# Kernel optimization log

Hardware: AMD Instinct MI355X
Metric: run time of the kernel (lower is better)

The kernel has to match this reference:

```python
import jax, jax.numpy as jnp
import numpy as np

B, D, T, H = 2048, 512, 16, 1024   # batch, covariate_dim, treatment_dim, mlp hidden
K, M = 50, 16                       # k_neighbors, manifold_dim


def _mlp(xt, W1, b1, W2, b2):
    # outcome model: [B, D+T] -> [B, 1]
    return jnp.tanh(xt @ W1 + b1) @ W2 + b2


def setup_inputs() -> dict:
    key = jax.random.key(0)
    k0, k1, k2, k3, k4 = jax.random.split(key, 5)
    x = jax.random.normal(k0, (B, D), dtype=jnp.float32)
    t = jax.random.normal(k1, (B, T), dtype=jnp.float32)
    perturbations = jax.random.normal(k2, (B, D), dtype=jnp.float32)
    W1 = jax.random.normal(k3, (D + T, H), dtype=jnp.float32) / np.float32(np.sqrt(D + T))
    b1 = jnp.zeros((H,), dtype=jnp.float32)
    W2 = jax.random.normal(k4, (H, 1), dtype=jnp.float32) / np.float32(np.sqrt(H))
    b2 = jnp.zeros((1,), dtype=jnp.float32)
    return {"x": x, "t": t, "perturbations": perturbations,
            "W1": W1, "b1": b1, "W2": W2, "b2": b2}


def reference(x, t, perturbations, W1, b1, W2, b2):
    # grad of sum(y) w.r.t. x (create_graph analog handled by composing jax.grad)
    def scalar_out(xx):
        return _mlp(jnp.concatenate([xx, t], axis=-1), W1, b1, W2, b2).sum()
    grad_x = jax.grad(scalar_out)(x)                      # [B, D]

    # kNN on perturbations (squared distances preserve topk-smallest ordering)
    sq = jnp.sum(perturbations * perturbations, axis=-1)  # [B]
    d2 = sq[:, None] + sq[None, :] - 2.0 * (perturbations @ perturbations.T)
    _, idx = jax.lax.top_k(-d2, K)                        # [B, K] nearest (incl. self)

    neigh = perturbations[idx]                            # [B, K, D] gather
    centered = neigh - neigh.mean(axis=1, keepdims=True)
    # batched reduced SVD: Vt has shape [B, min(K,D), D]
    _, _, Vt = jnp.linalg.svd(centered, full_matrices=False)
    basis = jnp.swapaxes(Vt[:, :M, :], 1, 2)              # [B, D, M] top-M right sing. vecs

    # projection of grad onto tangent space, summed squared norm
    coef = jnp.einsum('bdm,bd->bm', basis, grad_x)        # [B, M]
    proj = jnp.einsum('bdm,bm->bd', basis, coef)          # [B, D]
    return jnp.sum(proj * proj) / B
```

## Files before the change

### kernel.cpp

```cpp
#include <hip/hip_runtime.h>
#include <math.h>
#include <float.h>

#define B_ 2048
#define D_ 512
#define T_ 16
#define H_ 1024
#define K_ 50
#define M_ 16
#define NSWEEP 1
#define SX_STRIDE 2656
#define SLAB 128
#define SROW 136
#define FS 52

typedef __attribute__((ext_vector_type(8))) short s16x8;
typedef __attribute__((ext_vector_type(4))) float f32x4;
typedef __attribute__((ext_vector_type(2))) float f32x2;

#define GLL16(g, l) __builtin_amdgcn_global_load_lds( \
    (const __attribute__((address_space(1))) void*)(g), \
    (__attribute__((address_space(3))) void*)(l), 16, 0, 0)

__device__ __forceinline__ float bsum64(float v) {
  #pragma unroll
  for (int o = 1; o < 64; o <<= 1) v += __shfl_xor(v, o);
  return v;
}

__device__ __forceinline__ unsigned bf16_rne(float v) {
  union { float f; unsigned u; } a; a.f = v;
  return (a.u + 0x7FFFu + ((a.u >> 16) & 1u)) >> 16;
}
__device__ __forceinline__ float bf16_val(unsigned h) {
  union { unsigned u; float f; } a; a.u = h << 16;
  return a.f;
}
__device__ __forceinline__ void split_bf16(float v, unsigned short* h, unsigned short* l) {
  unsigned hh = bf16_rne(v);
  *h = (unsigned short)hh;
  *l = (unsigned short)bf16_rne(v - bf16_val(hh));
}

__global__ __launch_bounds__(256)
void prep_conv(const float* __restrict__ x, const float* __restrict__ t,
               const float* __restrict__ P, const float* __restrict__ W1,
               unsigned short* __restrict__ xh, unsigned short* __restrict__ xl,
               unsigned short* __restrict__ ph, unsigned short* __restrict__ pl,
               float* __restrict__ sq,
               unsigned short* __restrict__ th, unsigned short* __restrict__ tl,
               unsigned short* __restrict__ wh, unsigned short* __restrict__ wl,
               float* __restrict__ out) {
  __shared__ float tile[32][33];
  __shared__ float red[4];
  const int bid = blockIdx.x, tid = threadIdx.x;
  if (bid < B_) {
    const int b = bid;
    if (b == 0 && tid == 0) out[0] = 0.f;
    for (int c = tid; c < 544; c += 256) {
      float v = 0.f;
      if (c < 512) v = x[(size_t)b * 512 + c];
      else if (c < 528) v = t[(size_t)b * 16 + (c - 512)];
      unsigned short hh, ll; split_bf16(v, &hh, &ll);
      xh[(size_t)b * 544 + c] = hh;
      xl[(size_t)b * 544 + c] = ll;
    }
    float s = 0.f;
    for (int c = tid; c < 512; c += 256) {
      float v = P[(size_t)b * 512 + c];
      s += v * v;
      unsigned short hh, ll; split_bf16(v, &hh, &ll);
      ph[(size_t)b * 512 + c] = hh;
      pl[(size_t)b * 512 + c] = ll;
    }
    s = bsum64(s);
    if ((tid & 63) == 0) red[tid >> 6] = s;
    __syncthreads();
    if (tid == 0) sq[b] = (red[0] + red[1]) + (red[2] + red[3]);
  } else {
    const int cid = bid - B_;
    const int tx = tid & 31, ty = tid >> 5;
    const int kb = (cid % 17) * 32, hb = (cid / 17) * 32;
    #pragma unroll
    for (int j = 0; j < 4; j++) {
      int k = kb + ty + j * 8;
      float v = (k < 528) ? W1[(size_t)k * 1024 + hb + tx] : 0.f;
      tile[ty + j * 8][tx] = v;
      if (k < 528) {
        unsigned short hh, ll; split_bf16(v, &hh, &ll);
        wh[(size_t)k * 1024 + hb + tx] = hh;
        wl[(size_t)k * 1024 + hb + tx] = ll;
      }
    }
    __syncthreads();
    #pragma unroll
    for (int j = 0; j < 4; j++) {
      int hrow = hb + ty + j * 8;
      float v = tile[tx][ty + j * 8];
      unsigned short hh, ll; split_bf16(v, &hh, &ll);
      th[(size_t)hrow * 544 + kb + tx] = hh;
      tl[(size_t)hrow * 544 + kb + tx] = ll;
    }
  }
}

template <int EPI, int PASSES>
__global__ __launch_bounds__(256)
void mfma_nt(const unsigned short* __restrict__ Ah, const unsigned short* __restrict__ Al, int lda,
             const unsigned short* __restrict__ Bh, const unsigned short* __restrict__ Bl, int ldb,
             int K, float* __restrict__ C, int ldc,
             const float* __restrict__ b1, const float* __restrict__ W2,
             unsigned short* __restrict__ acth, unsigned short* __restrict__ actl) {
  __shared__ unsigned short sAh[2 * 2048], sBh[2 * 2048];
  __shared__ unsigned short sAl[PASSES == 3 ? 2 * 2048 : 16];
  __shared__ unsigned short sBl[PASSES == 3 ? 2 * 2048 : 16];
  const int tid = threadIdx.x;
  const int lane = tid & 63, wv = tid >> 6;
  const int wm = wv >> 1, wn = wv & 1;
  const int lr = lane & 15, lq = lane >> 4;
  const int m0 = blockIdx.y * 64, n0 = blockIdx.x * 64;
  const int srow = wv * 16 + (lane >> 2);
  const int sx = (srow & 3) ^ ((srow >> 2) & 3);
  const int gch = ((lane & 3) ^ sx) * 8;
  const size_t rowA = (size_t)(m0 + srow) * lda + gch;
  const size_t rowB = (size_t)(n0 + srow) * ldb + gch;

  f32x4 acc[2][2];
  #pragma unroll
  for (int mt = 0; mt < 2; mt++)
    #pragma unroll
    for (int nt = 0; nt < 2; nt++)
      #pragma unroll
      for (int i = 0; i < 4; i++) acc[mt][nt][i] = 0.f;

  auto STAGE = [&](int bufi, int kb) {
    const int off = bufi * 2048 + wv * 512;
    GLL16(Ah + rowA + kb, &sAh[off]);
    GLL16(Bh + rowB + kb, &sBh[off]);
    if (PASSES == 3) {
      GLL16(Al + rowA + kb, &sAl[off]);
      GLL16(Bl + rowB + kb, &sBl[off]);
    }
  };

  auto COMPUTE = [&](int bufi) {
    const int bo = bufi * 2048;
    s16x8 fah[2], fal[2], fbh[2], fbl[2];
    #pragma unroll
    for (int mt = 0; mt < 2; mt++) {
      const int r = wm * 32 + mt * 16 + lr;
      const int xo = (lq ^ ((r & 3) ^ ((r >> 2) & 3))) * 8;
      fah[mt] = *(const s16x8*)&sAh[bo + r * 32 + xo];
      if (PASSES == 3) fal[mt] = *(const s16x8*)&sAl[bo + r * 32 + xo];
    }
    #pragma unroll
    for (int nt = 0; nt < 2; nt++) {
      const int r = wn * 32 + nt * 16 + lr;
      const int xo = (lq ^ ((r & 3) ^ ((r >> 2) & 3))) * 8;
      fbh[nt] = *(const s16x8*)&sBh[bo + r * 32 + xo];
      if (PASSES == 3) fbl[nt] = *(const s16x8*)&sBl[bo + r * 32 + xo];
    }
    #pragma unroll
    for (int mt = 0; mt < 2; mt++)
      #pragma unroll
      for (int nt = 0; nt < 2; nt++)
        acc[mt][nt] = __builtin_amdgcn_mfma_f32_16x16x32_bf16(fah[mt], fbh[nt], acc[mt][nt], 0, 0, 0);
    if (PASSES == 3) {
      #pragma unroll
      for (int mt = 0; mt < 2; mt++)
        #pragma unroll
        for (int nt = 0; nt < 2; nt++)
          acc[mt][nt] = __builtin_amdgcn_mfma_f32_16x16x32_bf16(fah[mt], fbl[nt], acc[mt][nt], 0, 0, 0);
      #pragma unroll
      for (int mt = 0; mt < 2; mt++)
        #pragma unroll
        for (int nt = 0; nt < 2; nt++)
          acc[mt][nt] = __builtin_amdgcn_mfma_f32_16x16x32_bf16(fal[mt], fbh[nt], acc[mt][nt], 0, 0, 0);
    }
  };

  STAGE(0, 0);
  __syncthreads();
  int cur = 0;
  for (int kb = 32; kb < K; kb += 32) {
    STAGE(cur ^ 1, kb);
    COMPUTE(cur);
    __syncthreads();
    cur ^= 1;
  }
  COMPUTE(cur);

  #pragma unroll
  for (int nt = 0; nt < 2; nt++) {
    const int n = n0 + wn * 32 + nt * 16 + lr;
    float bb = 0.f, ww = 0.f;
    if (EPI == 1) { bb = b1[n]; ww = W2[n]; }
    #pragma unroll
    for (int mt = 0; mt < 2; mt++) {
      #pragma unroll
      for (int r = 0; r < 4; r++) {
        const int m = m0 + wm * 32 + mt * 16 + lq * 4 + r;
        float v = acc[mt][nt][r];
        if (EPI == 0) {
          C[(size_t)m * ldc + n] = v;
        } else if (EPI == 1) {
          float z = v + bb;
          float e = __builtin_amdgcn_exp2f(fabsf(z) * -2.885390082f);
          float rc = __builtin_amdgcn_rcpf(1.f + e);
          float s = 4.f * e * rc * rc * ww;
          unsigned short hh, ll; split_bf16(s, &hh, &ll);
          acth[(size_t)m * ldc + n] = hh;
          actl[(size_t)m * ldc + n] = ll;
        } else {
          unsigned short hh, ll; split_bf16(v, &hh, &ll);
          acth[(size_t)m * ldc + n] = hh;
          actl[(size_t)m * ldc + n] = ll;
        }
      }
    }
  }
}

__global__ __launch_bounds__(256)
void sbuild_kernel(const unsigned short* __restrict__ ph, const unsigned short* __restrict__ pl,
                   const unsigned short* __restrict__ gh, const unsigned short* __restrict__ gl,
                   const int* __restrict__ idx, float* __restrict__ Sx) {
  __shared__ unsigned short sh[64 * SROW];
  __shared__ unsigned short sl[64 * SROW];
  __shared__ int ids[K_];
  const int b = blockIdx.x;
  const int tid = threadIdx.x;
  if (tid < K_) ids[tid] = idx[b * K_ + tid];
  const int lane = tid & 63, wv = tid >> 6;
  const int wm = wv >> 1, wn = wv & 1;
  const int lr = lane & 15, lq = lane >> 4;
  const int strow = tid >> 4, stk = (tid & 15) * 8;
  __syncthreads();

  f32x4 acc[2][2];
  #pragma unroll
  for (int mt = 0; mt < 2; mt++)
    #pragma unroll
    for (int nt = 0; nt < 2; nt++)
      #pragma unroll
      for (int i = 0; i < 4; i++) acc[mt][nt][i] = 0.f;

  for (int kb = 0; kb < 512; kb += SLAB) {
    __syncthreads();
    #pragma unroll
    for (int p = 0; p < 4; p++) {
      const int r = p * 16 + strow;
      if (r < 51) {
        const unsigned short* srch = (r < 50) ? ph + (size_t)ids[r] * 512 : gh + (size_t)b * 512;
        const unsigned short* srcl = (r < 50) ? pl + (size_t)ids[r] * 512 : gl + (size_t)b * 512;
        *(float4*)&sh[r * SROW + stk] = *(const float4*)(srch + kb + stk);
        *(float4*)&sl[r * SROW + stk] = *(const float4*)(srcl + kb + stk);
      }
    }
    __syncthreads();
    #pragma unroll
    for (int kk = 0; kk < SLAB; kk += 32) {
      s16x8 fah[2], fal[2], fbh[2], fbl[2];
      #pragma unroll
      for (int mt = 0; mt < 2; mt++) {
        const int r = wm * 32 + mt * 16 + lr;
        fah[mt] = *(const s16x8*)&sh[r * SROW + kk + lq * 8];
        fal[mt] = *(const s16x8*)&sl[r * SROW + kk + lq * 8];
      }
      #pragma unroll
      for (int nt = 0; nt < 2; nt++) {
        const int r = wn * 32 + nt * 16 + lr;
        fbh[nt] = *(const s16x8*)&sh[r * SROW + kk + lq * 8];
        fbl[nt] = *(const s16x8*)&sl[r * SROW + kk + lq * 8];
      }
      #pragma unroll
      for (int mt = 0; mt < 2; mt++)
        #pragma unroll
        for (int nt = 0; nt < 2; nt++)
          acc[mt][nt] = __builtin_amdgcn_mfma_f32_16x16x32_bf16(fah[mt], fbh[nt], acc[mt][nt], 0, 0, 0);
      #pragma unroll
      for (int mt = 0; mt < 2; mt++)
        #pragma unroll
        for (int nt = 0; nt < 2; nt++)
          acc[mt][nt] = __builtin_amdgcn_mfma_f32_16x16x32_bf16(fah[mt], fbl[nt], acc[mt][nt], 0, 0, 0);
      #pragma unroll
      for (int mt = 0; mt < 2; mt++)
        #pragma unroll
        for (int nt = 0; nt < 2; nt++)
          acc[mt][nt] = __builtin_amdgcn_mfma_f32_16x16x32_bf16(fal[mt], fbh[nt], acc[mt][nt], 0, 0, 0);
    }
  }

  float* Sb = Sx + (size_t)b * SX_STRIDE;
  #pragma unroll
  for (int nt = 0; nt < 2; nt++) {
    const int n = wn * 32 + nt * 16 + lr;
    #pragma unroll
    for (int mt = 0; mt < 2; mt++) {
      #pragma unroll
      for (int r = 0; r < 4; r++) {
        const int m = wm * 32 + mt * 16 + lq * 4 + r;
        if (m < 51 && n < 52) Sb[m * 52 + n] = acc[mt][nt][r];
      }
    }
  }
}

__device__ __forceinline__ unsigned fkey(float f) {
  unsigned u = __float_as_uint(f);
  return u ^ ((unsigned)((int)u >> 31) | 0x80000000u);
}

__global__ __launch_bounds__(64)
void topk_kernel(const float* __restrict__ G, const float* __restrict__ sq,
                 int* __restrict__ idx) {
  const int b = blockIdx.x, lane = threadIdx.x;
  const float* row = G + (size_t)b * 2048;
  unsigned k[32];
  #pragma unroll
  for (int i = 0; i < 32; i++) {
    const int j = i * 64 + lane;
    k[i] = fkey(sq[j] - 2.f * row[j]);
  }
  unsigned V = 0;
  bool exact = false;
  for (int bit = 31; bit >= 0; bit--) {
    const unsigned cand = V | (1u << bit);
    int cnt = 0;
    #pragma unroll
    for (int i = 0; i < 32; i++) cnt += (k[i] < cand) ? 1 : 0;
    #pragma unroll
    for (int o = 1; o < 64; o <<= 1) cnt += __shfl_xor(cnt, o);
    if (cnt == K_) { V = cand; exact = true; break; }
    if (cnt < K_ + 1) V = cand;
  }
  int base = 0;
  #pragma unroll
  for (int i = 0; i < 32; i++) {
    const bool p = (k[i] < V);
    const unsigned long long mask = __ballot(p);
    if (p) {
      const int pos = base + __popcll(mask & ((1ull << lane) - 1ull));
      idx[b * K_ + pos] = i * 64 + lane;
    }
    base += __popcll(mask);
  }
  if (!exact && base < K_) {
    #pragma unroll
    for (int i = 0; i < 32; i++) {
      if (base >= K_) break;
      const bool p = (k[i] == V);
      const unsigned long long mask = __ballot(p);
      if (p) {
        const int pos = base + __popcll(mask & ((1ull << lane) - 1ull));
        if (pos < K_) idx[b * K_ + pos] = i * 64 + lane;
      }
      base += __popcll(mask);
    }
  }
}

__global__ __launch_bounds__(64, 2)
void final_kernel(const float* __restrict__ Sx, float* __restrict__ out) {
  __shared__ float cols[64 * FS];
  const int b = blockIdx.x;
  const int lane = threadIdx.x;
  const float* Sb = Sx + (size_t)b * SX_STRIDE;
  const bool act = lane < K_;

  float q = act ? Sb[50 * 52 + lane] : 0.f;
  float qm = bsum64(q) * (1.f / K_);
  float w = act ? (q - qm) : 0.f;

  f32x2 f2[25];
  #pragma unroll
  for (int i = 0; i < 25; i++) {
    f2[i].x = act ? Sb[(2 * i) * 52 + lane] : 0.f;
    f2[i].y = act ? Sb[(2 * i + 1) * 52 + lane] : 0.f;
  }

  float cm = 0.f;
  #pragma unroll
  for (int i = 0; i < 25; i++) cm += f2[i].x + f2[i].y;
  cm *= (1.f / K_);
  float gs = bsum64(act ? cm : 0.f) * (1.f / K_);
  float cs = cm - gs;
  #pragma unroll
  for (int i = 0; i < 25; i++) {
    float r0 = __shfl(cm, 2 * i);
    float r1 = __shfl(cm, 2 * i + 1);
    if (act) { f2[i].x -= r0 + cs; f2[i].y -= r1 + cs; }
  }

  float nrm = 0.f;
  #pragma unroll
  for (int i = 0; i < 25; i++) nrm += f2[i].x * f2[i].x + f2[i].y * f2[i].y;

  f32x4 f4[13];
  #pragma unroll
  for (int k = 0; k < 12; k++) {
    f4[k].x = f2[2 * k].x;     f4[k].y = f2[2 * k].y;
    f4[k].z = f2[2 * k + 1].x; f4[k].w = f2[2 * k + 1].y;
  }
  f4[12].x = f2[24].x; f4[12].y = f2[24].y; f4[12].z = nrm; f4[12].w = w;

  float* my = &cols[lane * FS];
  if (act) {
    #pragma unroll
    for (int k = 0; k < 13; k++) *(f32x4*)&my[4 * k] = f4[k];
  }

  for (int sweep = 0; sweep < NSWEEP; sweep++) {
    int mm = (lane == 0) ? 0 : 49 - lane;
    int kkv = 0;
    for (int r = 0; r < 49; r++) {
      if (act) {
        int m = mm;
        if (lane == kkv) m = 49;
        if (lane == 49)  m = kkv;

        const float* pc = &cols[m * FS];
        f32x4 y4[13];
        #pragma unroll
        for (int k = 0; k < 13; k++) y4[k] = *(const f32x4*)&pc[4 * k];
        const float onrm = y4[12].z;
        const float yw   = y4[12].w;

        f32x4 acc4 = {0.f, 0.f, 0.f, 0.f};
        #pragma unroll
        for (int k = 0; k < 12; k++) acc4 = __builtin_elementwise_fma(f4[k], y4[k], acc4);
        acc4.x = fmaf(f4[12].x, y4[12].x, acc4.x);
        acc4.y = fmaf(f4[12].y, y4[12].y, acc4.y);
        const float dot = (acc4.x + acc4.y) + (acc4.z + acc4.w);

        const bool isp = lane < m;
        float alpha = isp ? nrm : onrm;
        float beta  = isp ? onrm : nrm;
        float tau = (beta - alpha) * 0.5f * __builtin_amdgcn_rcpf(dot);
        float sg = (tau >= 0.f) ? 1.f : -1.f;
        float s1 = __builtin_amdgcn_sqrtf(1.f + tau * tau);
        float tt = sg * __builtin_amdgcn_rcpf(fabsf(tau) + s1);
        float cc = __builtin_amdgcn_rsqf(1.f + tt * tt);
        float ssv = tt * cc;
        float sr = isp ? -ssv : ssv;
        if (fabsf(dot) < 1e-20f) { cc = 1.f; sr = 0.f; }

        f32x4 c4 = {cc, cc, cc, cc};
        f32x4 s4 = {sr, sr, sr, sr};
        #pragma unroll
        for (int k = 0; k < 13; k++)
          f4[k] = __builtin_elementwise_fma(c4, f4[k], s4 * y4[k]);
        w = cc * w + sr * yw;
        nrm = cc * cc * nrm + sr * sr * onrm + 2.f * cc * sr * dot;
        f4[12].z = nrm;
        f4[12].w = w;

        #pragma unroll
        for (int k = 0; k < 13; k++) *(f32x4*)&my[4 * k] = f4[k];
      }
      mm = (mm == 48) ? 0 : mm + 1;
      kkv += 25; if (kkv >= 49) kkv -= 49;
    }
  }

  float n2 = 0.f;
  #pragma unroll
  for (int k = 0; k < 12; k++)
    n2 += f4[k].x * f4[k].x + f4[k].y * f4[k].y + f4[k].z * f4[k].z + f4[k].w * f4[k].w;
  n2 += f4[12].x * f4[12].x + f4[12].y * f4[12].y;
  int rank = 0;
  #pragma unroll
  for (int j = 0; j < K_; j++) {
    float vj = __shfl(n2, j);
    rank += (vj > n2 || (vj == n2 && j < lane)) ? 1 : 0;
  }
  float lam = sqrtf(n2);
  float contrib = (act && rank < M_) ? (w * w / lam) : 0.f;
  contrib = bsum64(contrib);
  if (lane == 0) atomicAdd(out, contrib * (1.f / B_));
}

extern "C" void kernel_launch(void* const* d_in, const int* in_sizes, int n_in,
                              void* d_out, int out_size, void* d_ws, size_t ws_size,
                              hipStream_t stream) {
  const float* x  = (const float*)d_in[0];
  const float* t  = (const float*)d_in[1];
  const float* P  = (const float*)d_in[2];
  const float* W1 = (const float*)d_in[3];
  const float* b1 = (const float*)d_in[4];
  const float* W2 = (const float*)d_in[5];
  float* out = (float*)d_out;

  float* G    = (float*)d_ws;
  float* Sx   = (float*)d_ws;
  unsigned short* xt_h  = (unsigned short*)(G + (size_t)B_ * B_);
  unsigned short* xt_l  = xt_h  + (size_t)B_ * 544;
  unsigned short* w1t_h = xt_l  + (size_t)B_ * 544;
  unsigned short* w1t_l = w1t_h + (size_t)H_ * 544;
  unsigned short* w1_h  = w1t_l + (size_t)H_ * 544;
  unsigned short* w1_l  = w1_h  + (size_t)528 * H_;
  unsigned short* p_h   = w1_l  + (size_t)528 * H_;
  unsigned short* p_l   = p_h   + (size_t)B_ * D_;
  unsigned short* act_h = p_l   + (size_t)B_ * D_;
  unsigned short* act_l = act_h + (size_t)B_ * H_;
  unsigned short* g_h   = act_l + (size_t)B_ * H_;
  unsigned short* g_l   = g_h   + (size_t)B_ * D_;
  float* sq   = (float*)(g_l + (size_t)B_ * D_);
  int*   idx  = (int*)(sq + B_);

  prep_conv<<<B_ + 544, 256, 0, stream>>>(x, t, P, W1, xt_h, xt_l, p_h, p_l, sq,
                                          w1t_h, w1t_l, w1_h, w1_l, out);

  mfma_nt<1, 3><<<dim3(H_ / 64, B_ / 64), 256, 0, stream>>>(
      xt_h, xt_l, 544, w1t_h, w1t_l, 544, 544,
      nullptr, H_, b1, W2, act_h, act_l);
  mfma_nt<2, 3><<<dim3(D_ / 64, B_ / 64), 256, 0, stream>>>(
      act_h, act_l, H_, w1_h, w1_l, H_, H_,
      nullptr, D_, nullptr, nullptr, g_h, g_l);
  mfma_nt<0, 1><<<dim3(B_ / 64, B_ / 64), 256, 0, stream>>>(
      p_h, nullptr, D_, p_h, nullptr, D_, D_,
      G, B_, nullptr, nullptr, nullptr, nullptr);

  topk_kernel<<<B_, 64, 0, stream>>>(G, sq, idx);
  sbuild_kernel<<<B_, 256, 0, stream>>>(p_h, p_l, g_h, g_l, idx, Sx);
  final_kernel<<<B_, 64, 0, stream>>>(Sx, out);
}
```

Baseline: 247.9 us.

## Fuse top-k into final kernel and gather Gram entries from full 3-pass P·Pᵀ

```diff
diff --git a/kernel.cpp b/kernel.cpp
--- a/kernel.cpp
+++ b/kernel.cpp
@@ -9,9 +9,6 @@
 #define K_ 50
 #define M_ 16
 #define NSWEEP 1
-#define SX_STRIDE 2656
-#define SLAB 128
-#define SROW 136
 #define FS 52
 
 typedef __attribute__((ext_vector_type(8))) short s16x8;
@@ -104,13 +101,14 @@
   }
 }
 
-template <int EPI, int PASSES>
+template <int EPI, int PASSES, int DUAL>
 __global__ __launch_bounds__(256)
 void mfma_nt(const unsigned short* __restrict__ Ah, const unsigned short* __restrict__ Al, int lda,
              const unsigned short* __restrict__ Bh, const unsigned short* __restrict__ Bl, int ldb,
              int K, float* __restrict__ C, int ldc,
              const float* __restrict__ b1, const float* __restrict__ W2,
-             unsigned short* __restrict__ acth, unsigned short* __restrict__ actl) {
+             unsigned short* __restrict__ acth, unsigned short* __restrict__ actl,
+             float* __restrict__ C1) {
   __shared__ unsigned short sAh[2 * 2048], sBh[2 * 2048];
   __shared__ unsigned short sAl[PASSES == 3 ? 2 * 2048 : 16];
   __shared__ unsigned short sBl[PASSES == 3 ? 2 * 2048 : 16];
@@ -126,12 +124,21 @@
   const size_t rowB = (size_t)(n0 + srow) * ldb + gch;
 
   f32x4 acc[2][2];
+  f32x4 acc1[DUAL ? 2 : 1][DUAL ? 2 : 1];
   #pragma unroll
   for (int mt = 0; mt < 2; mt++)
     #pragma unroll
     for (int nt = 0; nt < 2; nt++)
       #pragma unroll
       for (int i = 0; i < 4; i++) acc[mt][nt][i] = 0.f;
+  if (DUAL) {
+    #pragma unroll
+    for (int mt = 0; mt < 2; mt++)
+      #pragma unroll
+      for (int nt = 0; nt < 2; nt++)
+        #pragma unroll
+        for (int i = 0; i < 4; i++) acc1[mt][nt][i] = 0.f;
+  }
 
   auto STAGE = [&](int bufi, int kb) {
     const int off = bufi * 2048 + wv * 512;
@@ -165,6 +172,13 @@
       #pragma unroll
       for (int nt = 0; nt < 2; nt++)
         acc[mt][nt] = __builtin_amdgcn_mfma_f32_16x16x32_bf16(fah[mt], fbh[nt], acc[mt][nt], 0, 0, 0);
+    if (DUAL) {
+      #pragma unroll
+      for (int mt = 0; mt < 2; mt++)
+        #pragma unroll
+        for (int nt = 0; nt < 2; nt++)
+          acc1[mt][nt] = __builtin_amdgcn_mfma_f32_16x16x32_bf16(fah[mt], fbh[nt], acc1[mt][nt], 0, 0, 0);
+    }
     if (PASSES == 3) {
       #pragma unroll
       for (int mt = 0; mt < 2; mt++)
@@ -203,6 +217,7 @@
         float v = acc[mt][nt][r];
         if (EPI == 0) {
           C[(size_t)m * ldc + n] = v;
+          if (DUAL) C1[(size_t)m * ldc + n] = acc1[mt][nt][r];
         } else if (EPI == 1) {
           float z = v + bb;
           float e = __builtin_amdgcn_exp2f(fabsf(z) * -2.885390082f);
@@ -211,96 +226,7 @@
           unsigned short hh, ll; split_bf16(s, &hh, &ll);
           acth[(size_t)m * ldc + n] = hh;
           actl[(size_t)m * ldc + n] = ll;
-        } else {
-          unsigned short hh, ll; split_bf16(v, &hh, &ll);
-          acth[(size_t)m * ldc + n] = hh;
-          actl[(size_t)m * ldc + n] = ll;
         }
-      }
-    }
-  }
-}
-
-__global__ __launch_bounds__(256)
-void sbuild_kernel(const unsigned short* __restrict__ ph, const unsigned short* __restrict__ pl,
-                   const unsigned short* __restrict__ gh, const unsigned short* __restrict__ gl,
-                   const int* __restrict__ idx, float* __restrict__ Sx) {
-  __shared__ unsigned short sh[64 * SROW];
-  __shared__ unsigned short sl[64 * SROW];
-  __shared__ int ids[K_];
-  const int b = blockIdx.x;
-  const int tid = threadIdx.x;
-  if (tid < K_) ids[tid] = idx[b * K_ + tid];
-  const int lane = tid & 63, wv = tid >> 6;
-  const int wm = wv >> 1, wn = wv & 1;
-  const int lr = lane & 15, lq = lane >> 4;
-  const int strow = tid >> 4, stk = (tid & 15) * 8;
-  __syncthreads();
-
-  f32x4 acc[2][2];
-  #pragma unroll
-  for (int mt = 0; mt < 2; mt++)
-    #pragma unroll
-    for (int nt = 0; nt < 2; nt++)
-      #pragma unroll
-      for (int i = 0; i < 4; i++) acc[mt][nt][i] = 0.f;
-
-  for (int kb = 0; kb < 512; kb += SLAB) {
-    __syncthreads();
-    #pragma unroll
-    for (int p = 0; p < 4; p++) {
-      const int r = p * 16 + strow;
-      if (r < 51) {
-        const unsigned short* srch = (r < 50) ? ph + (size_t)ids[r] * 512 : gh + (size_t)b * 512;
-        const unsigned short* srcl = (r < 50) ? pl + (size_t)ids[r] * 512 : gl + (size_t)b * 512;
-        *(float4*)&sh[r * SROW + stk] = *(const float4*)(srch + kb + stk);
-        *(float4*)&sl[r * SROW + stk] = *(const float4*)(srcl + kb + stk);
-      }
-    }
-    __syncthreads();
-    #pragma unroll
-    for (int kk = 0; kk < SLAB; kk += 32) {
-      s16x8 fah[2], fal[2], fbh[2], fbl[2];
-      #pragma unroll
-      for (int mt = 0; mt < 2; mt++) {
-        const int r = wm * 32 + mt * 16 + lr;
-        fah[mt] = *(const s16x8*)&sh[r * SROW + kk + lq * 8];
-        fal[mt] = *(const s16x8*)&sl[r * SROW + kk + lq * 8];
-      }
-      #pragma unroll
-      for (int nt = 0; nt < 2; nt++) {
-        const int r = wn * 32 + nt * 16 + lr;
-        fbh[nt] = *(const s16x8*)&sh[r * SROW + kk + lq * 8];
-        fbl[nt] = *(const s16x8*)&sl[r * SROW + kk + lq * 8];
-      }
-      #pragma unroll
-      for (int mt = 0; mt < 2; mt++)
-        #pragma unroll
-        for (int nt = 0; nt < 2; nt++)
-          acc[mt][nt] = __builtin_amdgcn_mfma_f32_16x16x32_bf16(fah[mt], fbh[nt], acc[mt][nt], 0, 0, 0);
-      #pragma unroll
-      for (int mt = 0; mt < 2; mt++)
-        #pragma unroll
-        for (int nt = 0; nt < 2; nt++)
-          acc[mt][nt] = __builtin_amdgcn_mfma_f32_16x16x32_bf16(fah[mt], fbl[nt], acc[mt][nt], 0, 0, 0);
-      #pragma unroll
-      for (int mt = 0; mt < 2; mt++)
-        #pragma unroll
-        for (int nt = 0; nt < 2; nt++)
-          acc[mt][nt] = __builtin_amdgcn_mfma_f32_16x16x32_bf16(fal[mt], fbh[nt], acc[mt][nt], 0, 0, 0);
-    }
-  }
-
-  float* Sb = Sx + (size_t)b * SX_STRIDE;
-  #pragma unroll
-  for (int nt = 0; nt < 2; nt++) {
-    const int n = wn * 32 + nt * 16 + lr;
-    #pragma unroll
-    for (int mt = 0; mt < 2; mt++) {
-      #pragma unroll
-      for (int r = 0; r < 4; r++) {
-        const int m = wm * 32 + mt * 16 + lq * 4 + r;
-        if (m < 51 && n < 52) Sb[m * 52 + n] = acc[mt][nt][r];
       }
     }
   }
@@ -311,16 +237,29 @@
   return u ^ ((unsigned)((int)u >> 31) | 0x80000000u);
 }
 
-__global__ __launch_bounds__(64)
-void topk_kernel(const float* __restrict__ G, const float* __restrict__ sq,
-                 int* __restrict__ idx) {
-  const int b = blockIdx.x, lane = threadIdx.x;
-  const float* row = G + (size_t)b * 2048;
-  unsigned k[32];
+__global__ __launch_bounds__(64, 2)
+void final_kernel(const float* __restrict__ G1, const float* __restrict__ G3,
+                  const float* __restrict__ sq,
+                  const float* __restrict__ P, const float* __restrict__ g32,
+                  float* __restrict__ out) {
+  __shared__ float cols[64 * FS];
+  __shared__ float gld[512];
+  __shared__ int ids[64];
+  const int b = blockIdx.x;
+  const int lane = threadIdx.x;
+
+  {
+    const float4* grow = (const float4*)(g32 + (size_t)b * 512);
+    ((float4*)gld)[lane] = grow[lane];
+    ((float4*)gld)[lane + 64] = grow[lane + 64];
+  }
+
+  const float* row = G1 + (size_t)b * 2048;
+  unsigned kk[32];
   #pragma unroll
   for (int i = 0; i < 32; i++) {
     const int j = i * 64 + lane;
-    k[i] = fkey(sq[j] - 2.f * row[j]);
+    kk[i] = fkey(sq[j] - 2.f * row[j]);
   }
   unsigned V = 0;
   bool exact = false;
@@ -328,7 +267,7 @@
     const unsigned cand = V | (1u << bit);
     int cnt = 0;
     #pragma unroll
-    for (int i = 0; i < 32; i++) cnt += (k[i] < cand) ? 1 : 0;
+    for (int i = 0; i < 32; i++) cnt += (kk[i] < cand) ? 1 : 0;
     #pragma unroll
     for (int o = 1; o < 64; o <<= 1) cnt += __shfl_xor(cnt, o);
     if (cnt == K_) { V = cand; exact = true; break; }
@@ -337,11 +276,11 @@
   int base = 0;
   #pragma unroll
   for (int i = 0; i < 32; i++) {
-    const bool p = (k[i] < V);
+    const bool p = (kk[i] < V);
     const unsigned long long mask = __ballot(p);
     if (p) {
       const int pos = base + __popcll(mask & ((1ull << lane) - 1ull));
-      idx[b * K_ + pos] = i * 64 + lane;
+      ids[pos] = i * 64 + lane;
     }
     base += __popcll(mask);
   }
@@ -349,34 +288,42 @@
     #pragma unroll
     for (int i = 0; i < 32; i++) {
       if (base >= K_) break;
-      const bool p = (k[i] == V);
+      const bool p = (kk[i] == V);
       const unsigned long long mask = __ballot(p);
       if (p) {
         const int pos = base + __popcll(mask & ((1ull << lane) - 1ull));
-        if (pos < K_) idx[b * K_ + pos] = i * 64 + lane;
+        if (pos < K_) ids[pos] = i * 64 + lane;
       }
       base += __popcll(mask);
     }
   }
-}
-
-__global__ __launch_bounds__(64, 2)
-void final_kernel(const float* __restrict__ Sx, float* __restrict__ out) {
-  __shared__ float cols[64 * FS];
-  const int b = blockIdx.x;
-  const int lane = threadIdx.x;
-  const float* Sb = Sx + (size_t)b * SX_STRIDE;
+
   const bool act = lane < K_;
-
-  float q = act ? Sb[50 * 52 + lane] : 0.f;
-  float qm = bsum64(q) * (1.f / K_);
+  const int mycol = act ? ids[lane] : 0;
+
+  float q = 0.f;
+  if (act) {
+    const float4* Pr = (const float4*)(P + (size_t)mycol * 512);
+    f32x4 qa = {0.f, 0.f, 0.f, 0.f};
+    #pragma unroll 4
+    for (int c = 0; c < 128; c++) {
+      float4 pv = Pr[c];
+      float4 gv = ((const float4*)gld)[c];
+      qa.x = fmaf(gv.x, pv.x, qa.x);
+      qa.y = fmaf(gv.y, pv.y, qa.y);
+      qa.z = fmaf(gv.z, pv.z, qa.z);
+      qa.w = fmaf(gv.w, pv.w, qa.w);
+    }
+    q = (qa.x + qa.y) + (qa.z + qa.w);
+  }
+  float qm = bsum64(act ? q : 0.f) * (1.f / K_);
   float w = act ? (q - qm) : 0.f;
 
   f32x2 f2[25];
   #pragma unroll
   for (int i = 0; i < 25; i++) {
-    f2[i].x = act ? Sb[(2 * i) * 52 + lane] : 0.f;
-    f2[i].y = act ? Sb[(2 * i + 1) * 52 + lane] : 0.f;
+    f2[i].x = act ? G3[(size_t)ids[2 * i] * 2048 + mycol] : 0.f;
+    f2[i].y = act ? G3[(size_t)ids[2 * i + 1] * 2048 + mycol] : 0.f;
   }
 
   float cm = 0.f;
@@ -491,9 +438,10 @@
   const float* W2 = (const float*)d_in[5];
   float* out = (float*)d_out;
 
-  float* G    = (float*)d_ws;
-  float* Sx   = (float*)d_ws;
-  unsigned short* xt_h  = (unsigned short*)(G + (size_t)B_ * B_);
+  float* G3   = (float*)d_ws;
+  unsigned short* act_h = (unsigned short*)(G3 + (size_t)B_ * B_);
+  unsigned short* act_l = act_h + (size_t)B_ * H_;
+  unsigned short* xt_h  = act_l + (size_t)B_ * H_;
   unsigned short* xt_l  = xt_h  + (size_t)B_ * 544;
   unsigned short* w1t_h = xt_l  + (size_t)B_ * 544;
   unsigned short* w1t_l = w1t_h + (size_t)H_ * 544;
@@ -501,27 +449,22 @@
   unsigned short* w1_l  = w1_h  + (size_t)528 * H_;
   unsigned short* p_h   = w1_l  + (size_t)528 * H_;
   unsigned short* p_l   = p_h   + (size_t)B_ * D_;
-  unsigned short* act_h = p_l   + (size_t)B_ * D_;
-  unsigned short* act_l = act_h + (size_t)B_ * H_;
-  unsigned short* g_h   = act_l + (size_t)B_ * H_;
-  unsigned short* g_l   = g_h   + (size_t)B_ * D_;
-  float* sq   = (float*)(g_l + (size_t)B_ * D_);
-  int*   idx  = (int*)(sq + B_);
+  float* g32  = (float*)(p_l + (size_t)B_ * D_);
+  float* sq   = g32 + (size_t)B_ * D_;
+  float* G1   = (float*)act_h;
 
   prep_conv<<<B_ + 544, 256, 0, stream>>>(x, t, P, W1, xt_h, xt_l, p_h, p_l, sq,
                                           w1t_h, w1t_l, w1_h, w1_l, out);
 
-  mfma_nt<1, 3><<<dim3(H_ / 64, B_ / 64), 256, 0, stream>>>(
+  mfma_nt<1, 3, 0><<<dim3(H_ / 64, B_ / 64), 256, 0, stream>>>(
       xt_h, xt_l, 544, w1t_h, w1t_l, 544, 544,
-      nullptr, H_, b1, W2, act_h, act_l);
-  mfma_nt<2, 3><<<dim3(D_ / 64, B_ / 64), 256, 0, stream>>>(
+      nullptr, H_, b1, W2, act_h, act_l, nullptr);
+  mfma_nt<0, 3, 0><<<dim3(D_ / 64, B_ / 64), 256, 0, stream>>>(
       act_h, act_l, H_, w1_h, w1_l, H_, H_,
-      nullptr, D_, nullptr, nullptr, g_h, g_l);
-  mfma_nt<0, 1><<<dim3(B_ / 64, B_ / 64), 256, 0, stream>>>(
-      p_h, nullptr, D_, p_h, nullptr, D_, D_,
-      G, B_, nullptr, nullptr, nullptr, nullptr);
-
-  topk_kernel<<<B_, 64, 0, stream>>>(G, sq, idx);
-  sbuild_kernel<<<B_, 256, 0, stream>>>(p_h, p_l, g_h, g_l, idx, Sx);
-  final_kernel<<<B_, 64, 0, stream>>>(Sx, out);
-}
+      g32, D_, nullptr, nullptr, nullptr, nullptr, nullptr);
+  mfma_nt<0, 3, 1><<<dim3(B_ / 64, B_ / 64), 256, 0, stream>>>(
+      p_h, p_l, D_, p_h, p_l, D_, D_,
+      G3, B_, nullptr, nullptr, nullptr, nullptr, G1);
+
+  final_kernel<<<B_, 64, 0, stream>>>(G1, G3, sq, P, g32, out);
+}
```

New measurement: 245.3 us. No clear change (-1.0%).

## Merge independent activation GEMM and Gram GEMM into one launch

Applied to the files above, without the earlier changes.

```diff
diff --git a/kernel.cpp b/kernel.cpp
--- a/kernel.cpp
+++ b/kernel.cpp
@@ -105,20 +105,19 @@
 }
 
 template <int EPI, int PASSES>
-__global__ __launch_bounds__(256)
-void mfma_nt(const unsigned short* __restrict__ Ah, const unsigned short* __restrict__ Al, int lda,
-             const unsigned short* __restrict__ Bh, const unsigned short* __restrict__ Bl, int ldb,
-             int K, float* __restrict__ C, int ldc,
-             const float* __restrict__ b1, const float* __restrict__ W2,
-             unsigned short* __restrict__ acth, unsigned short* __restrict__ actl) {
-  __shared__ unsigned short sAh[2 * 2048], sBh[2 * 2048];
-  __shared__ unsigned short sAl[PASSES == 3 ? 2 * 2048 : 16];
-  __shared__ unsigned short sBl[PASSES == 3 ? 2 * 2048 : 16];
+__device__ __forceinline__
+void gemm_tile(const unsigned short* __restrict__ Ah, const unsigned short* __restrict__ Al, int lda,
+               const unsigned short* __restrict__ Bh, const unsigned short* __restrict__ Bl, int ldb,
+               int K, float* __restrict__ C, int ldc,
+               const float* __restrict__ b1, const float* __restrict__ W2,
+               unsigned short* __restrict__ acth, unsigned short* __restrict__ actl,
+               int m0, int n0,
+               unsigned short* sAh, unsigned short* sBh,
+               unsigned short* sAl, unsigned short* sBl) {
   const int tid = threadIdx.x;
   const int lane = tid & 63, wv = tid >> 6;
   const int wm = wv >> 1, wn = wv & 1;
   const int lr = lane & 15, lq = lane >> 4;
-  const int m0 = blockIdx.y * 64, n0 = blockIdx.x * 64;
   const int srow = wv * 16 + (lane >> 2);
   const int sx = (srow & 3) ^ ((srow >> 2) & 3);
   const int gch = ((lane & 3) ^ sx) * 8;
@@ -222,6 +221,41 @@
 }
 
 __global__ __launch_bounds__(256)
+void gemm_actG(const unsigned short* __restrict__ xt_h, const unsigned short* __restrict__ xt_l,
+               const unsigned short* __restrict__ w1t_h, const unsigned short* __restrict__ w1t_l,
+               const float* __restrict__ b1, const float* __restrict__ W2,
+               unsigned short* __restrict__ act_h, unsigned short* __restrict__ act_l,
+               const unsigned short* __restrict__ p_h, float* __restrict__ G) {
+  __shared__ unsigned short sAh[2 * 2048], sBh[2 * 2048];
+  __shared__ unsigned short sAl[2 * 2048], sBl[2 * 2048];
+  const int bid = blockIdx.x;
+  if (bid < 512) {
+    const int n0 = (bid & 15) * 64, m0 = (bid >> 4) * 64;
+    gemm_tile<1, 3>(xt_h, xt_l, 544, w1t_h, w1t_l, 544, 544,
+                    nullptr, H_, b1, W2, act_h, act_l, m0, n0,
+                    sAh, sBh, sAl, sBl);
+  } else {
+    const int idx = bid - 512;
+    const int n0 = (idx & 31) * 64, m0 = (idx >> 5) * 64;
+    gemm_tile<0, 1>(p_h, nullptr, D_, p_h, nullptr, D_, D_,
+                    G, B_, nullptr, nullptr, nullptr, nullptr, m0, n0,
+                    sAh, sBh, sAl, sBl);
+  }
+}
+
+__global__ __launch_bounds__(256)
+void mfma_grad(const unsigned short* __restrict__ act_h, const unsigned short* __restrict__ act_l,
+               const unsigned short* __restrict__ w1_h, const unsigned short* __restrict__ w1_l,
+               unsigned short* __restrict__ g_h, unsigned short* __restrict__ g_l) {
+  __shared__ unsigned short sAh[2 * 2048], sBh[2 * 2048];
+  __shared__ unsigned short sAl[2 * 2048], sBl[2 * 2048];
+  const int n0 = (blockIdx.x & 7) * 64, m0 = (blockIdx.x >> 3) * 64;
+  gemm_tile<2, 3>(act_h, act_l, H_, w1_h, w1_l, H_, H_,
+                  nullptr, D_, nullptr, nullptr, g_h, g_l, m0, n0,
+                  sAh, sBh, sAl, sBl);
+}
+
+__global__ __launch_bounds__(256)
 void sbuild_kernel(const unsigned short* __restrict__ ph, const unsigned short* __restrict__ pl,
                    const unsigned short* __restrict__ gh, const unsigned short* __restrict__ gl,
                    const int* __restrict__ idx, float* __restrict__ Sx) {
@@ -511,15 +545,10 @@
   prep_conv<<<B_ + 544, 256, 0, stream>>>(x, t, P, W1, xt_h, xt_l, p_h, p_l, sq,
                                           w1t_h, w1t_l, w1_h, w1_l, out);
 
-  mfma_nt<1, 3><<<dim3(H_ / 64, B_ / 64), 256, 0, stream>>>(
-      xt_h, xt_l, 544, w1t_h, w1t_l, 544, 544,
-      nullptr, H_, b1, W2, act_h, act_l);
-  mfma_nt<2, 3><<<dim3(D_ / 64, B_ / 64), 256, 0, stream>>>(
-      act_h, act_l, H_, w1_h, w1_l, H_, H_,
-      nullptr, D_, nullptr, nullptr, g_h, g_l);
-  mfma_nt<0, 1><<<dim3(B_ / 64, B_ / 64), 256, 0, stream>>>(
-      p_h, nullptr, D_, p_h, nullptr, D_, D_,
-      G, B_, nullptr, nullptr, nullptr, nullptr);
+  gemm_actG<<<1536, 256, 0, stream>>>(xt_h, xt_l, w1t_h, w1t_l, b1, W2,
+                                      act_h, act_l, p_h, G);
+
+  mfma_grad<<<256, 256, 0, stream>>>(act_h, act_l, w1_h, w1_l, g_h, g_l);
 
   topk_kernel<<<B_, 64, 0, stream>>>(G, sq, idx);
   sbuild_kernel<<<B_, 256, 0, stream>>>(p_h, p_l, g_h, g_l, idx, Sx);
```

After: 244.4 us. About the same (-1.4%).
